# Kernel tuning notes

Hardware: AMD Instinct MI355X
Metric: run time of the kernel (lower is better)

Reference implementation:

```python
import jax, jax.numpy as jnp
import numpy as np

E = 1024
H = 16
D = E // H
MLP = 4096
EPS = 1e-5


def _layernorm(x, g, b):
    mu = jnp.mean(x, axis=-1, keepdims=True)
    var = jnp.mean(jnp.square(x - mu), axis=-1, keepdims=True)
    return (x - mu) * jax.lax.rsqrt(var + EPS) * g + b


def setup_inputs() -> dict:
    key = jax.random.key(0)
    ks = jax.random.split(key, 10)
    s = lambda fan_in: 1.0 / np.sqrt(fan_in)
    return {
        "x": jax.random.normal(ks[0], (4, 2048, E), dtype=jnp.float32),
        "qkv_w": jax.random.uniform(ks[1], (3 * E, E), jnp.float32, -s(E), s(E)),
        "fc_w": jax.random.uniform(ks[2], (E, E), jnp.float32, -s(E), s(E)),
        "fc_b": jax.random.uniform(ks[3], (E,), jnp.float32, -s(E), s(E)),
        "ln1_g": jnp.ones((E,), jnp.float32),
        "ln1_b": jnp.zeros((E,), jnp.float32),
        "ln2_g": jnp.ones((E,), jnp.float32),
        "ln2_b": jnp.zeros((E,), jnp.float32),
        "w1": jax.random.uniform(ks[4], (MLP, E), jnp.float32, -s(E), s(E)),
        "b1": jax.random.uniform(ks[5], (MLP,), jnp.float32, -s(E), s(E)),
        "w2": jax.random.uniform(ks[6], (E, MLP), jnp.float32, -s(MLP), s(MLP)),
        "b2": jax.random.uniform(ks[7], (E,), jnp.float32, -s(MLP), s(MLP)),
    }


def reference(x, qkv_w, fc_w, fc_b, ln1_g, ln1_b, ln2_g, ln2_b, w1, b1, w2, b2):
    B, S, _ = x.shape
    scale = D ** (-0.5)
    # --- attention sublayer ---
    h = _layernorm(x, ln1_g, ln1_b)
    qkv = (h @ qkv_w.T).reshape(B, S, 3, H, D)
    q, k, v = jnp.moveaxis(qkv, 2, 0)            # each [B, S, H, D]
    q = q.transpose(0, 2, 1, 3)                  # [B, H, S, D]
    k = k.transpose(0, 2, 1, 3)
    v = v.transpose(0, 2, 1, 3)
    scores = jnp.einsum("bhqd,bhkd->bhqk", q, k) * scale
    attn = jax.nn.softmax(scores, axis=-1)
    out = jnp.einsum("bhqk,bhkd->bhqd", attn, v)
    out = out.transpose(0, 2, 1, 3).reshape(B, S, E)
    x = x + (out @ fc_w.T + fc_b)
    # --- MLP sublayer ---
    h = _layernorm(x, ln2_g, ln2_b)
    h = jax.nn.gelu(h @ w1.T + b1, approximate=False)
    x = x + (h @ w2.T + b2)
    return x
```

## Files before the change

### kernel.cpp

```cpp
#include <hip/hip_runtime.h>
#include <cstdint>
#include <cmath>

#define EDIM 1024
#define SEQ 2048
#define BATCH 4
#define NHEAD 16
#define HDIM 64
#define MLPD 4096
#define ROWS 8192

typedef unsigned short u16;
typedef __attribute__((ext_vector_type(8))) short short8;
typedef __attribute__((ext_vector_type(4))) float floatx4;

#define AS1 __attribute__((address_space(1)))
#define AS3 __attribute__((address_space(3)))

#define Q_SCALE 0.18033688011112042f

__device__ __forceinline__ void async16(const void* g, void* l) {
  __builtin_amdgcn_global_load_lds((AS1 void*)g, (AS3 void*)l, 16, 0, 0);
}

__device__ __forceinline__ u16 f2bf(float f) {
  union { float f; unsigned int u; } v; v.f = f;
  unsigned int u = v.u;
  u += 0x7fffu + ((u >> 16) & 1u);
  return (u16)(u >> 16);
}

__device__ __forceinline__ unsigned int u32of(float f) {
  union { float f; unsigned int u; } v; v.f = f; return v.u;
}

__device__ __forceinline__ unsigned int pack_trunc(float a, float b) {
  return __builtin_amdgcn_perm(u32of(b), u32of(a), 0x07060302u);
}

__device__ __forceinline__ float exp2_fast(float x) {
  return __builtin_amdgcn_exp2f(x);
}

__device__ __forceinline__ float gelu_f(float x) {
  const float y = 0.7978845608028654f * (x + 0.044715f * x * x * x);
  const float e = exp2_fast(y * 2.885390081777927f);
  const float t = 1.0f - 2.0f * __builtin_amdgcn_rcpf(1.0f + e);
  return 0.5f * x * (1.0f + t);
}

__global__ __launch_bounds__(256) void cvt_all(const float* __restrict__ a, u16* __restrict__ oa, int na,
                                               const float* __restrict__ b, u16* __restrict__ ob, int nb,
                                               const float* __restrict__ c, u16* __restrict__ oc, int nc,
                                               const float* __restrict__ d, u16* __restrict__ od) {
  int i = (blockIdx.x * 256 + threadIdx.x) * 4;
  const float* src;
  u16* dst;
  if (i < na) { src = a; dst = oa; }
  else if ((i -= na) < nb) { src = b; dst = ob; }
  else if ((i -= nb) < nc) { src = c; dst = oc; }
  else { i -= nc; src = d; dst = od; }
  const float4 v = *(const float4*)(src + i);
  dst[i + 0] = f2bf(v.x); dst[i + 1] = f2bf(v.y);
  dst[i + 2] = f2bf(v.z); dst[i + 3] = f2bf(v.w);
}

__global__ __launch_bounds__(256) void ln_bf16(const float* __restrict__ x,
                                               const float* __restrict__ g,
                                               const float* __restrict__ bta,
                                               u16* __restrict__ outp) {
  const int row = blockIdx.x;
  const int tid = threadIdx.x;
  const float4 v = *(const float4*)(x + (size_t)row * EDIM + tid * 4);
  float s = v.x + v.y + v.z + v.w;
  float ss = v.x * v.x + v.y * v.y + v.z * v.z + v.w * v.w;
#pragma unroll
  for (int o = 1; o < 64; o <<= 1) {
    s += __shfl_xor(s, o);
    ss += __shfl_xor(ss, o);
  }
  __shared__ float red[8];
  const int wave = tid >> 6, lane = tid & 63;
  if (lane == 0) { red[wave] = s; red[4 + wave] = ss; }
  __syncthreads();
  s = red[0] + red[1] + red[2] + red[3];
  ss = red[4] + red[5] + red[6] + red[7];
  const float mu = s * (1.0f / 1024.0f);
  const float var = ss * (1.0f / 1024.0f) - mu * mu;
  const float inv = rsqrtf(var + 1e-5f);
  const float4 gv = *(const float4*)(g + tid * 4);
  const float4 bv = *(const float4*)(bta + tid * 4);
  u16* od = outp + (size_t)row * EDIM + tid * 4;
  od[0] = f2bf((v.x - mu) * inv * gv.x + bv.x);
  od[1] = f2bf((v.y - mu) * inv * gv.y + bv.y);
  od[2] = f2bf((v.z - mu) * inv * gv.z + bv.z);
  od[3] = f2bf((v.w - mu) * inv * gv.w + bv.w);
}

template <int EPI, int BM = 256>
__global__ __launch_bounds__(512) void gemm_bt(const u16* __restrict__ A,
                                               const u16* __restrict__ Bw,
                                               void* __restrict__ Cout,
                                               const float* __restrict__ bias,
                                               const float* __restrict__ res,
                                               int M, int N, int K) {
  constexpr int IB = BM / 64;
  constexpr int WROWS = BM / 4;
  __shared__ __align__(16) u16 As[BM * 64];
  __shared__ __align__(16) u16 Bs[128 * 64];
  const int tid = threadIdx.x;
  const int lane = tid & 63;
  const int wave = tid >> 6;
  const int quad = lane >> 4;
  const int cl = lane & 15;
  const int row0 = blockIdx.y * BM;
  const int col0 = blockIdx.x * 128;
  const int wm = wave >> 1;
  const int wn = wave & 1;

  floatx4 acc[IB][4];
#pragma unroll
  for (int i = 0; i < IB; ++i)
#pragma unroll
    for (int j = 0; j < 4; ++j) acc[i][j] = (floatx4){0.f, 0.f, 0.f, 0.f};

  const int trow = tid >> 3;
  const int gc = (tid & 7) ^ (trow & 7);
  const u16* Ath = A + (size_t)(row0 + trow) * K + gc * 8;
  const u16* Bth = Bw + (size_t)(col0 + trow) * K + gc * 8;
  u16* lA = As + tid * 8;
  u16* lB = Bs + tid * 8;
  const size_t pstride = (size_t)64 * K;

  for (int k0 = 0; k0 < K; k0 += 64) {
    __syncthreads();
#pragma unroll
    for (int p = 0; p < BM / 64; ++p)
      async16(Ath + p * pstride + k0, lA + p * 4096);
#pragma unroll
    for (int p = 0; p < 2; ++p)
      async16(Bth + p * pstride + k0, lB + p * 4096);
    __syncthreads();
#pragma unroll
    for (int s = 0; s < 2; ++s) {
      const int ko = ((s * 4 + quad) ^ (cl & 7)) * 8;
      short8 af[IB], bfr[4];
#pragma unroll
      for (int i = 0; i < IB; ++i)
        af[i] = *(const short8*)(As + (wm * WROWS + i * 16 + cl) * 64 + ko);
#pragma unroll
      for (int j = 0; j < 4; ++j)
        bfr[j] = *(const short8*)(Bs + (wn * 64 + j * 16 + cl) * 64 + ko);
#pragma unroll
      for (int i = 0; i < IB; ++i)
#pragma unroll
        for (int j = 0; j < 4; ++j)
          acc[i][j] = __builtin_amdgcn_mfma_f32_16x16x32_bf16(af[i], bfr[j], acc[i][j], 0, 0, 0);
    }
  }

  const float qscale = (EPI == 5 && col0 < 1024) ? Q_SCALE : 1.0f;
#pragma unroll
  for (int i = 0; i < IB; ++i) {
#pragma unroll
    for (int r = 0; r < 4; ++r) {
      const int row = row0 + wm * WROWS + i * 16 + quad * 4 + r;
#pragma unroll
      for (int j = 0; j < 4; ++j) {
        const int col = col0 + wn * 64 + j * 16 + cl;
        const size_t idx = (size_t)row * N + col;
        float v = acc[i][j][r];
        if (EPI == 0) {
          ((float*)Cout)[idx] = v;
        } else if (EPI == 1 || EPI == 3) {
          ((float*)Cout)[idx] = v + bias[col] + res[idx];
        } else if (EPI == 2) {
          ((u16*)Cout)[idx] = f2bf(gelu_f(v + bias[col]));
        } else if (EPI == 4) {
          ((u16*)Cout)[idx] = f2bf(v);
        } else if (EPI == 5) {
          ((u16*)Cout)[idx] = f2bf(v * qscale);
        }
      }
    }
  }
}

template <int EPI, int BN>
__global__ __launch_bounds__(512, 2) void gemm8(const u16* __restrict__ A,
                                                const u16* __restrict__ Bw,
                                                void* __restrict__ Cout,
                                                const float* __restrict__ bias,
                                                const float* __restrict__ res,
                                                int M, int N, int K) {
  constexpr int BHALF = BN / 128;
  constexpr int REG = 2 + BHALF;
  constexpr int NF = BN / 64;
  constexpr int DBS = REG * 8192;
  __shared__ __align__(16) u16 lds[2 * REG * 8192];

  const int tid = threadIdx.x;
  const int lane = tid & 63;
  const int wave = tid >> 6;
  const int quad = lane >> 4;
  const int cl = lane & 15;
  const int wm = wave >> 2;
  const int wn = wave & 3;
  const int row0 = blockIdx.y * 256;
  const int col0 = blockIdx.x * BN;

  const int trow = tid >> 3;
  const int gc = (tid & 7) ^ (trow & 7);
  const size_t aoff = (size_t)(row0 + trow) * K + gc * 8;
  const size_t boff = (size_t)(col0 + trow) * K + gc * 8;
  const size_t rstride = (size_t)128 * K;
  const size_t hstride = (size_t)64 * K;

  const int aro = wm * 8192 + cl * 64;
  const int bro = (BN == 256) ? ((2 + (wn >> 1)) * 8192 + ((wn & 1) * 64 + cl) * 64)
                              : (2 * 8192 + (wn * 32 + cl) * 64);
  const int ko0 = ((0 + quad) ^ (cl & 7)) * 8;
  const int ko1 = ((4 + quad) ^ (cl & 7)) * 8;

  floatx4 acc[8][NF];
#pragma unroll
  for (int i = 0; i < 8; ++i)
#pragma unroll
    for (int j = 0; j < NF; ++j) acc[i][j] = (floatx4){0.f, 0.f, 0.f, 0.f};

  const int nt = K >> 6;

#pragma unroll
  for (int r = 0; r < REG; ++r) {
    const u16* s0 = (r < 2) ? (A + aoff + (size_t)r * rstride)
                            : (Bw + boff + (size_t)(r - 2) * rstride);
    async16(s0, lds + r * 8192 + tid * 8);
    async16(s0 + hstride, lds + r * 8192 + 4096 + tid * 8);
  }
  asm volatile("s_waitcnt vmcnt(0)" ::: "memory");
  __builtin_amdgcn_s_barrier();
  __builtin_amdgcn_sched_barrier(0);

  short8 bf[NF][2];

  for (int t = 0; t < nt; ++t) {
    u16* cb = lds + (t & 1) * DBS;
    u16* nb = lds + ((t + 1) & 1) * DBS;
    const int kn = (t + 1) * 64;
    const bool more = (t + 1 < nt);
#pragma unroll
    for (int q = 0; q < 4; ++q) {
      short8 a00 = *(const short8*)(cb + aro + (2 * q + 0) * 1024 + ko0);
      short8 a01 = *(const short8*)(cb + aro + (2 * q + 0) * 1024 + ko1);
      short8 a10 = *(const short8*)(cb + aro + (2 * q + 1) * 1024 + ko0);
      short8 a11 = *(const short8*)(cb + aro + (2 * q + 1) * 1024 + ko1);
      if (q == 0) {
#pragma unroll
        for (int n = 0; n < NF; ++n) {
          bf[n][0] = *(const short8*)(cb + bro + n * 1024 + ko0);
          bf[n][1] = *(const short8*)(cb + bro + n * 1024 + ko1);
        }
      }
      if (q < REG && more) {
        const u16* s0 = (q < 2) ? (A + aoff + (size_t)q * rstride + kn)
                                : (Bw + boff + (size_t)(q - 2) * rstride + kn);
        async16(s0, nb + q * 8192 + tid * 8);
        async16(s0 + hstride, nb + q * 8192 + 4096 + tid * 8);
      }
      __builtin_amdgcn_s_barrier();
      asm volatile("s_waitcnt lgkmcnt(0)" ::: "memory");
      __builtin_amdgcn_sched_barrier(0);
      __builtin_amdgcn_s_setprio(1);
#pragma unroll
      for (int n = 0; n < NF; ++n) {
        acc[2 * q + 0][n] = __builtin_amdgcn_mfma_f32_16x16x32_bf16(a00, bf[n][0], acc[2 * q + 0][n], 0, 0, 0);
        acc[2 * q + 0][n] = __builtin_amdgcn_mfma_f32_16x16x32_bf16(a01, bf[n][1], acc[2 * q + 0][n], 0, 0, 0);
        acc[2 * q + 1][n] = __builtin_amdgcn_mfma_f32_16x16x32_bf16(a10, bf[n][0], acc[2 * q + 1][n], 0, 0, 0);
        acc[2 * q + 1][n] = __builtin_amdgcn_mfma_f32_16x16x32_bf16(a11, bf[n][1], acc[2 * q + 1][n], 0, 0, 0);
      }
      __builtin_amdgcn_s_setprio(0);
      if (q == 3) { asm volatile("s_waitcnt vmcnt(0)" ::: "memory"); }
      __builtin_amdgcn_s_barrier();
      __builtin_amdgcn_sched_barrier(0);
    }
  }

  const float qscale = (EPI == 5 && col0 < 1024) ? Q_SCALE : 1.0f;
#pragma unroll
  for (int i = 0; i < 8; ++i) {
#pragma unroll
    for (int r = 0; r < 4; ++r) {
      const int row = row0 + wm * 128 + i * 16 + quad * 4 + r;
#pragma unroll
      for (int j = 0; j < NF; ++j) {
        const int col = col0 + wn * (BN / 4) + j * 16 + cl;
        const size_t idx = (size_t)row * N + col;
        float v = acc[i][j][r];
        if (EPI == 0) {
          ((float*)Cout)[idx] = v;
        } else if (EPI == 1 || EPI == 3) {
          ((float*)Cout)[idx] = v + bias[col] + res[idx];
        } else if (EPI == 2) {
          ((u16*)Cout)[idx] = f2bf(gelu_f(v + bias[col]));
        } else if (EPI == 4) {
          ((u16*)Cout)[idx] = f2bf(v);
        } else if (EPI == 5) {
          ((u16*)Cout)[idx] = f2bf(v * qscale);
        }
      }
    }
  }
}

__global__ __launch_bounds__(256) void vtrans(const u16* __restrict__ qkv,
                                              u16* __restrict__ vt) {
  __shared__ unsigned int T[64 * 65];
  const int tid = threadIdx.x;
  const int bh = blockIdx.y;
  const int b = bh >> 4;
  const int h = bh & 15;
  const int s0 = blockIdx.x * 64;
#pragma unroll
  for (int pp = 0; pp < 2; ++pp) {
    const int g = pp * 256 + tid;
    const int r = g >> 3;
    const int d0 = (g & 7) * 8;
    const u16* src = qkv + (size_t)(b * SEQ + s0 + r) * 3072 + 2048 + h * 64 + d0;
    short8 v = *(const short8*)src;
#pragma unroll
    for (int i = 0; i < 8; ++i) T[(d0 + i) * 65 + r] = (u16)v[i];
  }
  __syncthreads();
#pragma unroll
  for (int pp = 0; pp < 2; ++pp) {
    const int g = pp * 256 + tid;
    const int d = g >> 3;
    const int sc = (g & 7) * 8;
    short8 v;
#pragma unroll
    for (int i = 0; i < 8; ++i) v[i] = (short)(u16)T[d * 65 + sc + i];
    *(short8*)(vt + ((size_t)bh * 64 + d) * SEQ + s0 + sc) = v;
  }
}

__global__ __launch_bounds__(256, 4) void attn3(const u16* __restrict__ qkv,
                                                const u16* __restrict__ vt,
                                                u16* __restrict__ outp) {
  __shared__ __align__(16) u16 smem[8192 + 8192 + 4 * 32 * 72];
  u16* Ks = smem;
  u16* Vs = smem + 8192;
  const int tid = threadIdx.x;
  const int lane = tid & 63;
  const int wave = tid >> 6;
  const int quad = lane >> 4;
  const int cl = lane & 15;

  const int f = blockIdx.y * 16 + blockIdx.x;
  const int xcd = f & 7;
  const int u = f >> 3;
  const int qi = u & 15;
  const int bh = xcd * 8 + (u >> 4);
  const int b = bh >> 4;
  const int h = bh & 15;
  const int q0 = qi * 128;
  u16* Pw = smem + 16384 + wave * (32 * 72);

  const u16* qbase = qkv + (size_t)(b * SEQ) * 3072 + h * 64;
  const u16* kbase = qbase + 1024;
  const u16* vbase = vt + (size_t)bh * 64 * SEQ;

#pragma unroll
  for (int p = 0; p < 4; ++p) {
    const int g = (wave * 4 + p) * 64 + lane;
    const int r = g >> 3;
    const int c = (g & 7) ^ (r & 7);
    async16(qbase + (size_t)(q0 + r) * 3072 + c * 8, smem + g * 8);
  }
  __syncthreads();
  short8 qf[2][2];
#pragma unroll
  for (int ng = 0; ng < 2; ++ng)
#pragma unroll
    for (int kc = 0; kc < 2; ++kc) {
      const int row = wave * 32 + ng * 16 + cl;
      qf[ng][kc] = *(const short8*)(smem + row * 64 + (((kc * 4 + quad) ^ (cl & 7)) * 8));
    }

  floatx4 O[4][2];
  float lrun[2] = {0.f, 0.f};
#pragma unroll
  for (int mg = 0; mg < 4; ++mg)
#pragma unroll
    for (int ng = 0; ng < 2; ++ng) O[mg][ng] = (floatx4){0.f, 0.f, 0.f, 0.f};

  for (int kt = 0; kt < SEQ / 128; ++kt) {
    const int k0 = kt * 128;
    __syncthreads();
    const u16* kb = kbase + (size_t)k0 * 3072;
#pragma unroll
    for (int p = 0; p < 2; ++p) {
      const int g = wave * 128 + p * 64 + lane;
      const int rk = g >> 3;
      const int ck = (g & 7) ^ (rk & 7);
      async16(kb + (size_t)rk * 3072 + ck * 8, Ks + g * 8);
      const int rv = g >> 4;
      const int cv = (g & 15) ^ (rv & 15);
      async16(vbase + (size_t)rv * SEQ + k0 + cv * 8, Vs + g * 8);
    }
    __syncthreads();

#pragma unroll
    for (int s = 0; s < 2; ++s) {
      floatx4 Sc[4][2];
#pragma unroll
      for (int mg = 0; mg < 4; ++mg)
#pragma unroll
        for (int ng = 0; ng < 2; ++ng) Sc[mg][ng] = (floatx4){0.f, 0.f, 0.f, 0.f};
#pragma unroll
      for (int kc = 0; kc < 2; ++kc) {
        short8 kf[4];
#pragma unroll
        for (int mg = 0; mg < 4; ++mg) {
          const int row = s * 64 + mg * 16 + cl;
          kf[mg] = *(const short8*)(Ks + row * 64 + (((kc * 4 + quad) ^ (cl & 7)) * 8));
        }
#pragma unroll
        for (int mg = 0; mg < 4; ++mg)
#pragma unroll
          for (int ng = 0; ng < 2; ++ng)
            Sc[mg][ng] = __builtin_amdgcn_mfma_f32_16x16x32_bf16(kf[mg], qf[ng][kc], Sc[mg][ng], 0, 0, 0);
      }

#pragma unroll
      for (int ng = 0; ng < 2; ++ng) {
        float rs = 0.f;
#pragma unroll
        for (int mg = 0; mg < 4; ++mg)
#pragma unroll
          for (int r = 0; r < 4; ++r) {
            const float pv = exp2_fast(Sc[mg][ng][r]);
            Sc[mg][ng][r] = pv;
            rs += pv;
          }
        rs += __shfl_xor(rs, 16);
        rs += __shfl_xor(rs, 32);
        lrun[ng] += rs;
      }

#pragma unroll
      for (int mg = 0; mg < 4; ++mg)
#pragma unroll
        for (int ng = 0; ng < 2; ++ng) {
          const unsigned int lo = pack_trunc(Sc[mg][ng][0], Sc[mg][ng][1]);
          const unsigned int hi = pack_trunc(Sc[mg][ng][2], Sc[mg][ng][3]);
          *(uint2*)(Pw + (ng * 16 + cl) * 72 + mg * 16 + quad * 4) = make_uint2(lo, hi);
        }

#pragma unroll
      for (int kc = 0; kc < 2; ++kc) {
        short8 pf[2], vf[4];
#pragma unroll
        for (int ng = 0; ng < 2; ++ng)
          pf[ng] = *(const short8*)(Pw + (ng * 16 + cl) * 72 + kc * 32 + quad * 8);
#pragma unroll
        for (int mg = 0; mg < 4; ++mg) {
          const int row = mg * 16 + cl;
          vf[mg] = *(const short8*)(Vs + row * 128 + (((s * 8 + kc * 4 + quad) ^ (cl & 15)) * 8));
        }
#pragma unroll
        for (int mg = 0; mg < 4; ++mg)
#pragma unroll
          for (int ng = 0; ng < 2; ++ng)
            O[mg][ng] = __builtin_amdgcn_mfma_f32_16x16x32_bf16(vf[mg], pf[ng], O[mg][ng], 0, 0, 0);
      }
    }
  }

#pragma unroll
  for (int ng = 0; ng < 2; ++ng) {
    const float inv = 1.0f / lrun[ng];
    const int qrow = q0 + wave * 32 + ng * 16 + cl;
    u16* od = outp + (size_t)(b * SEQ + qrow) * EDIM + h * 64;
#pragma unroll
    for (int mg = 0; mg < 4; ++mg) {
      const unsigned int lo = (unsigned int)f2bf(O[mg][ng][0] * inv) |
                              ((unsigned int)f2bf(O[mg][ng][1] * inv) << 16);
      const unsigned int hi = (unsigned int)f2bf(O[mg][ng][2] * inv) |
                              ((unsigned int)f2bf(O[mg][ng][3] * inv) << 16);
      *(uint2*)(od + mg * 16 + quad * 4) = make_uint2(lo, hi);
    }
  }
}

extern "C" void kernel_launch(void* const* d_in, const int* in_sizes, int n_in,
                              void* d_out, int out_size, void* d_ws, size_t ws_size,
                              hipStream_t stream) {
  const float* x    = (const float*)d_in[0];
  const float* qkvw = (const float*)d_in[1];
  const float* fcw  = (const float*)d_in[2];
  const float* fcb  = (const float*)d_in[3];
  const float* ln1g = (const float*)d_in[4];
  const float* ln1b = (const float*)d_in[5];
  const float* ln2g = (const float*)d_in[6];
  const float* ln2b = (const float*)d_in[7];
  const float* w1   = (const float*)d_in[8];
  const float* b1   = (const float*)d_in[9];
  const float* w2   = (const float*)d_in[10];
  const float* b2   = (const float*)d_in[11];

  char* ws = (char*)d_ws;
  size_t off = 0;
  u16* wqkv = (u16*)(ws + off); off += (size_t)3 * EDIM * EDIM * 2;
  u16* wfc  = (u16*)(ws + off); off += (size_t)EDIM * EDIM * 2;
  u16* w1b  = (u16*)(ws + off); off += (size_t)MLPD * EDIM * 2;
  u16* w2b  = (u16*)(ws + off); off += (size_t)EDIM * MLPD * 2;
  u16* hbuf = (u16*)(ws + off); off += (size_t)ROWS * EDIM * 2;
  u16* aout = (u16*)(ws + off); off += (size_t)ROWS * EDIM * 2;
  float* x2 = (float*)(ws + off); off += (size_t)ROWS * EDIM * 4;
  u16* qkvb = (u16*)(ws + off); off += (size_t)ROWS * 3 * EDIM * 2;
  u16* vtb  = (u16*)(ws + off); off += (size_t)ROWS * EDIM * 2;
  u16* hmlp = qkvb;

  cvt_all<<<12288, 256, 0, stream>>>(qkvw, wqkv, 3 * EDIM * EDIM,
                                     fcw, wfc, EDIM * EDIM,
                                     w1, w1b, MLPD * EDIM,
                                     w2, w2b);

  ln_bf16<<<ROWS, 256, 0, stream>>>(x, ln1g, ln1b, hbuf);
  gemm8<5, 256><<<dim3(12, 32), 512, 0, stream>>>(hbuf, wqkv, qkvb, nullptr, nullptr,
                                                  ROWS, 3 * EDIM, EDIM);
  vtrans<<<dim3(SEQ / 64, 64), 256, 0, stream>>>(qkvb, vtb);
  attn3<<<dim3(16, 64), 256, 0, stream>>>(qkvb, vtb, aout);
  gemm_bt<1, 128><<<dim3(8, 64), 512, 0, stream>>>(aout, wfc, x2, fcb, x,
                                                   ROWS, EDIM, EDIM);
  ln_bf16<<<ROWS, 256, 0, stream>>>(x2, ln2g, ln2b, hbuf);
  gemm8<2, 256><<<dim3(16, 32), 512, 0, stream>>>(hbuf, w1b, hmlp, b1, nullptr,
                                                  ROWS, MLPD, EDIM);
  gemm8<3, 128><<<dim3(8, 32), 512, 0, stream>>>(hmlp, w2b, (float*)d_out, b2, x2,
                                                 ROWS, EDIM, MLPD);
}
```

Measured before the change: 542.5 us.

## Remap GEMM blocks per XCD and issue all next-tile prefetches up front

Both GEMM kernels now remap the linear block index so that blocks landing on the same XCD (round-robin by index mod 8) work on a contiguous band of output rows. The aim is better L2 reuse of A and B tiles within each XCD. The pipelined GEMM also issues all async global-to-LDS loads for the next K tile in the first sub-step, not spreading them over the sub-steps, so memory latency has more time to hide. The remap assumes gridDim.y is divisible by 8, and the earlier burst of loads may contend with the LDS reads happening at the same time.

Measured after the change: 499.9 us. -7.9%, faster.

```diff
diff --git a/kernel.cpp b/kernel.cpp
--- a/kernel.cpp
+++ b/kernel.cpp
@@ -113,8 +113,17 @@
   const int wave = tid >> 6;
   const int quad = lane >> 4;
   const int cl = lane & 15;
-  const int row0 = blockIdx.y * BM;
-  const int col0 = blockIdx.x * 128;
+
+  const int nx = gridDim.x;
+  const int f = blockIdx.y * nx + blockIdx.x;
+  const int xcd = f & 7;
+  const int uu = f >> 3;
+  const int rows_per = gridDim.y >> 3;
+  const int bxy = xcd * rows_per + uu / nx;
+  const int bxx = uu % nx;
+
+  const int row0 = bxy * BM;
+  const int col0 = bxx * 128;
   const int wm = wave >> 1;
   const int wn = wave & 1;
 
@@ -206,8 +215,14 @@
   const int cl = lane & 15;
   const int wm = wave >> 2;
   const int wn = wave & 3;
-  const int row0 = blockIdx.y * 256;
-  const int col0 = blockIdx.x * BN;
+
+  const int nx = gridDim.x;
+  const int f = blockIdx.y * nx + blockIdx.x;
+  const int xcd = f & 7;
+  const int uu = f >> 3;
+  const int rows_per = gridDim.y >> 3;
+  const int row0 = (xcd * rows_per + uu / nx) * 256;
+  const int col0 = (uu % nx) * BN;
 
   const int trow = tid >> 3;
   const int gc = (tid & 7) ^ (trow & 7);
@@ -260,12 +275,15 @@
           bf[n][0] = *(const short8*)(cb + bro + n * 1024 + ko0);
           bf[n][1] = *(const short8*)(cb + bro + n * 1024 + ko1);
         }
-      }
-      if (q < REG && more) {
-        const u16* s0 = (q < 2) ? (A + aoff + (size_t)q * rstride + kn)
-                                : (Bw + boff + (size_t)(q - 2) * rstride + kn);
-        async16(s0, nb + q * 8192 + tid * 8);
-        async16(s0 + hstride, nb + q * 8192 + 4096 + tid * 8);
+        if (more) {
+#pragma unroll
+          for (int r = 0; r < REG; ++r) {
+            const u16* s0 = (r < 2) ? (A + aoff + (size_t)r * rstride + kn)
+                                    : (Bw + boff + (size_t)(r - 2) * rstride + kn);
+            async16(s0, nb + r * 8192 + tid * 8);
+            async16(s0 + hstride, nb + r * 8192 + 4096 + tid * 8);
+          }
+        }
       }
       __builtin_amdgcn_s_barrier();
       asm volatile("s_waitcnt lgkmcnt(0)" ::: "memory");
```
